# Kernel tuning notes

Hardware: AMD Instinct MI355X
Metric: run time of the kernel (lower is better)

## Reference

```python
import jax, jax.numpy as jnp
import numpy as np

H = 4096      # hidden_size (Llama-7B)
I = 11008     # intermediate_size (Llama-7B)
T = 4096      # tokens = batch 2 * seq 2048


def setup_inputs() -> dict:
    key = jax.random.key(0)
    ks = jax.random.split(key, 10)
    # int8 activations in [-128, 127]
    x = jax.random.randint(ks[0], (T, H), -128, 128, dtype=jnp.int32).astype(jnp.int8)
    # int4 weights stored as int8 values in [-8, 7], layout [out, in]
    gate_w = jax.random.randint(ks[1], (I, H), -8, 8, dtype=jnp.int32).astype(jnp.int8)
    up_w   = jax.random.randint(ks[2], (I, H), -8, 8, dtype=jnp.int32).astype(jnp.int8)
    down_w = jax.random.randint(ks[3], (H, I), -8, 8, dtype=jnp.int32).astype(jnp.int8)
    # per-output-channel dequant scale (input_scale * weight_scale) and fp32 bias
    gate_alpha = jax.random.uniform(ks[4], (I,), jnp.float32, 1e-4, 3e-4)
    up_alpha   = jax.random.uniform(ks[5], (I,), jnp.float32, 1e-4, 3e-4)
    down_alpha = jax.random.uniform(ks[6], (H,), jnp.float32, 1e-4, 3e-4)
    gate_bias = jax.random.normal(ks[7], (I,), jnp.float32) * 0.01
    up_bias   = jax.random.normal(ks[8], (I,), jnp.float32) * 0.01
    down_bias = jax.random.normal(ks[9], (H,), jnp.float32) * 0.01
    down_input_scale = jnp.array(0.1, dtype=jnp.float32)
    return dict(x=x, gate_w=gate_w, up_w=up_w, down_w=down_w,
                gate_alpha=gate_alpha, gate_bias=gate_bias,
                up_alpha=up_alpha, up_bias=up_bias,
                down_alpha=down_alpha, down_bias=down_bias,
                down_input_scale=down_input_scale)


def _w4a8_linear(x_i8, w_i4, alpha, bias):
    # int8 act x int4 weight -> int32 accumulate, per-out-channel dequant, fp32 out
    acc = jnp.matmul(x_i8.astype(jnp.int32), w_i4.T.astype(jnp.int32))  # [T, out]
    return acc.astype(jnp.float32) * alpha + bias


def reference(x, gate_w, up_w, down_w, gate_alpha, gate_bias, up_alpha, up_bias,
              down_alpha, down_bias, down_input_scale):
    g = _w4a8_linear(x, gate_w, gate_alpha, gate_bias)          # [T, I] fp32
    u = _w4a8_linear(x, up_w, up_alpha, up_bias)                # [T, I] fp32
    h = jax.nn.silu(g) * u                                      # SwiGLU
    # requantize to int8 for down_proj input (values kept exact as fp32)
    hq = jnp.clip(jnp.round(h / down_input_scale), -128.0, 127.0)
    out = jnp.matmul(hq, down_w.T.astype(jnp.float32)) * down_alpha + down_bias
    return out
```

## Files before the change

kernel.cpp:

```cpp
#include <hip/hip_runtime.h>
#include <stdint.h>

#define H_DIM 4096
#define I_DIM 11008
#define T_DIM 4096

typedef int i32x4 __attribute__((ext_vector_type(4)));
typedef const void __attribute__((address_space(1))) gvoid_t;
typedef void __attribute__((address_space(3))) svoid_t;

__device__ __forceinline__ void gload_lds16(const void* gsrc, void* ldst) {
    __builtin_amdgcn_global_load_lds((gvoid_t*)gsrc, (svoid_t*)ldst, 16, 0, 0);
}
__device__ __forceinline__ void wait_vmcnt6() {
    asm volatile("s_waitcnt vmcnt(6)" ::: "memory");
}
__device__ __forceinline__ void wait_vmcnt0() {
    asm volatile("s_waitcnt vmcnt(0)" ::: "memory");
}
__device__ __forceinline__ void wait_lgkm0() {
    asm volatile("s_waitcnt lgkmcnt(0)" ::: "memory");
    __builtin_amdgcn_sched_barrier(0);
}
__device__ __forceinline__ void barrier_() {
    asm volatile("s_barrier" ::: "memory");
}

__device__ __forceinline__ uint32_t pack4(int4 v) {
    uint32_t r = (uint32_t)(uint8_t)v.x;
    r |= (uint32_t)(uint8_t)v.y << 8;
    r |= (uint32_t)(uint8_t)v.z << 16;
    r |= (uint32_t)(uint8_t)v.w << 24;
    return r;
}

__global__ void convert_kernel(const int* __restrict__ src, int8_t* __restrict__ dst,
                               int n4) {
    int idx = blockIdx.x * blockDim.x + threadIdx.x;
    int stride = gridDim.x * blockDim.x;
    for (int i = idx; i < n4; i += stride) {
        int4 v = ((const int4*)src)[i];
        ((uint32_t*)dst)[i] = pack4(v);
    }
}

#define MFMA_I8 __builtin_amdgcn_mfma_i32_16x16x64_i8

__global__ __launch_bounds__(256, 2)
void gateup_kernel(const int8_t* __restrict__ x8, const int8_t* __restrict__ gw8,
                   const int8_t* __restrict__ uw8,
                   const float* __restrict__ galpha, const float* __restrict__ gbias,
                   const float* __restrict__ ualpha, const float* __restrict__ ubias,
                   const float* __restrict__ scale_p, int8_t* __restrict__ hq)
{
    __shared__ __align__(16) int8_t lsA[2][128 * 64];
    __shared__ __align__(16) int8_t lsG[2][128 * 64];
    __shared__ __align__(16) int8_t lsU[2][128 * 64];

    const int bid = blockIdx.x;
    const int mt = bid & 31;
    const int nt = bid >> 5;
    const int m0 = mt << 7;
    const int n0 = nt << 7;

    const int tid  = threadIdx.x;
    const int lane = tid & 63;
    const int wid  = tid >> 6;
    const int wr   = wid >> 1;
    const int wc   = wid & 1;
    const int lr   = lane & 15;
    const int rdsw = ((lane >> 4) ^ ((lr >> 1) & 3)) << 4;

    const int srow = tid >> 2;
    const int scol = ((tid & 3) ^ ((tid >> 3) & 3)) << 4;
    const int woff = wid << 10;

    const int8_t* As = x8  + (size_t)(m0 + srow) * H_DIM + scol;
    const int8_t* Gs = gw8 + (size_t)(n0 + srow) * H_DIM + scol;
    const int8_t* Us = uw8 + (size_t)(n0 + srow) * H_DIM + scol;

    i32x4 accg[4][4], accu[4][4];
#pragma unroll
    for (int mf = 0; mf < 4; ++mf)
#pragma unroll
        for (int nf = 0; nf < 4; ++nf) {
            accg[mf][nf] = i32x4{0, 0, 0, 0};
            accu[mf][nf] = i32x4{0, 0, 0, 0};
        }

    const int aro = (wr * 64 + lr) * 64 + rdsw;
    const int gro = (wc * 64 + lr) * 64 + rdsw;

#define STAGE_GU(b, kb) do { \
        gload_lds16(As + (kb),                        &lsA[b][woff]); \
        gload_lds16(As + (kb) + (size_t)64 * H_DIM,   &lsA[b][4096 + woff]); \
        gload_lds16(Gs + (kb),                        &lsG[b][woff]); \
        gload_lds16(Gs + (kb) + (size_t)64 * H_DIM,   &lsG[b][4096 + woff]); \
        gload_lds16(Us + (kb),                        &lsU[b][woff]); \
        gload_lds16(Us + (kb) + (size_t)64 * H_DIM,   &lsU[b][4096 + woff]); \
    } while (0)

    const int NKT = H_DIM / 64;
    STAGE_GU(0, 0);
    STAGE_GU(1, 64);

    for (int t = 0; t < NKT; ++t) {
        const int cur = t & 1;
        wait_vmcnt6();
        barrier_();
        i32x4 af[4], bg[4], bu[4];
#pragma unroll
        for (int mf = 0; mf < 4; ++mf) af[mf] = *(const i32x4*)&lsA[cur][aro + mf * 1024];
#pragma unroll
        for (int nf = 0; nf < 4; ++nf) {
            bg[nf] = *(const i32x4*)&lsG[cur][gro + nf * 1024];
            bu[nf] = *(const i32x4*)&lsU[cur][gro + nf * 1024];
        }
        wait_lgkm0();
        barrier_();
        {
            const int t2 = (t + 2 < NKT) ? (t + 2) : (t + 2 - NKT);
            STAGE_GU(cur, t2 * 64);
        }
#pragma unroll
        for (int mf = 0; mf < 4; ++mf)
#pragma unroll
            for (int nf = 0; nf < 4; ++nf) {
                accg[mf][nf] = MFMA_I8(af[mf], bg[nf], accg[mf][nf], 0, 0, 0);
                accu[mf][nf] = MFMA_I8(af[mf], bu[nf], accu[mf][nf], 0, 0, 0);
            }
    }
#undef STAGE_GU
    wait_vmcnt0();

    const float scale = *scale_p;
#pragma unroll
    for (int nf = 0; nf < 4; ++nf) {
        const int col = n0 + wc * 64 + nf * 16 + lr;
        const float gA = galpha[col], gB = gbias[col];
        const float uA = ualpha[col], uB = ubias[col];
#pragma unroll
        for (int mf = 0; mf < 4; ++mf) {
            const int row0 = m0 + wr * 64 + mf * 16 + (lane >> 4) * 4;
#pragma unroll
            for (int j = 0; j < 4; ++j) {
                float g = (float)accg[mf][nf][j] * gA + gB;
                float u = (float)accu[mf][nf][j] * uA + uB;
                float s = 1.0f / (1.0f + __expf(-g));
                float h = g * s * u;
                float q = rintf(h / scale);
                q = fminf(127.0f, fmaxf(-128.0f, q));
                hq[(size_t)(row0 + j) * I_DIM + col] = (int8_t)q;
            }
        }
    }
}

__global__ __launch_bounds__(256, 2)
void down_kernel(const int8_t* __restrict__ hq, const int8_t* __restrict__ dw8,
                 const float* __restrict__ dalpha, const float* __restrict__ dbias,
                 float* __restrict__ out)
{
    __shared__ __align__(16) int8_t lsA[2][256 * 64];
    __shared__ __align__(16) int8_t lsB[2][128 * 64];

    const int bid = blockIdx.x;
    const int mt = bid & 15;
    const int nt = bid >> 4;
    const int m0 = mt << 8;
    const int n0 = nt << 7;

    const int tid  = threadIdx.x;
    const int lane = tid & 63;
    const int wid  = tid >> 6;
    const int wr   = wid >> 1;
    const int wc   = wid & 1;
    const int lr   = lane & 15;
    const int rdsw = ((lane >> 4) ^ ((lr >> 1) & 3)) << 4;

    const int srow = tid >> 2;
    const int scol = ((tid & 3) ^ ((tid >> 3) & 3)) << 4;
    const int woff = wid << 10;

    const int8_t* Ap = hq  + (size_t)(m0 + srow) * I_DIM + scol;
    const int8_t* Bp = dw8 + (size_t)(n0 + srow) * I_DIM + scol;

    i32x4 acc[8][4];
#pragma unroll
    for (int mf = 0; mf < 8; ++mf)
#pragma unroll
        for (int nf = 0; nf < 4; ++nf) acc[mf][nf] = i32x4{0, 0, 0, 0};

    const int aro = (wr * 128 + lr) * 64 + rdsw;
    const int bro = (wc * 64 + lr) * 64 + rdsw;

#define STAGE_D(b, kb) do { \
        gload_lds16(Ap + (kb),                         &lsA[b][woff]); \
        gload_lds16(Ap + (kb) + (size_t)64 * I_DIM,    &lsA[b][4096 + woff]); \
        gload_lds16(Ap + (kb) + (size_t)128 * I_DIM,   &lsA[b][8192 + woff]); \
        gload_lds16(Ap + (kb) + (size_t)192 * I_DIM,   &lsA[b][12288 + woff]); \
        gload_lds16(Bp + (kb),                         &lsB[b][woff]); \
        gload_lds16(Bp + (kb) + (size_t)64 * I_DIM,    &lsB[b][4096 + woff]); \
    } while (0)

    const int NKT = I_DIM / 64;
    STAGE_D(0, 0);
    STAGE_D(1, 64);

    for (int t = 0; t < NKT; ++t) {
        const int cur = t & 1;
        wait_vmcnt6();
        barrier_();
        i32x4 af[8], bf[4];
#pragma unroll
        for (int mf = 0; mf < 8; ++mf) af[mf] = *(const i32x4*)&lsA[cur][aro + mf * 1024];
#pragma unroll
        for (int nf = 0; nf < 4; ++nf) bf[nf] = *(const i32x4*)&lsB[cur][bro + nf * 1024];
        wait_lgkm0();
        barrier_();
        {
            const int t2 = (t + 2 < NKT) ? (t + 2) : (t + 2 - NKT);
            STAGE_D(cur, t2 * 64);
        }
#pragma unroll
        for (int mf = 0; mf < 8; ++mf)
#pragma unroll
            for (int nf = 0; nf < 4; ++nf)
                acc[mf][nf] = MFMA_I8(af[mf], bf[nf], acc[mf][nf], 0, 0, 0);
    }
#undef STAGE_D
    wait_vmcnt0();

#pragma unroll
    for (int nf = 0; nf < 4; ++nf) {
        const int col = n0 + wc * 64 + nf * 16 + lr;
        const float dA = dalpha[col], dB = dbias[col];
#pragma unroll
        for (int mf = 0; mf < 8; ++mf) {
            const int row0 = m0 + wr * 128 + mf * 16 + (lane >> 4) * 4;
#pragma unroll
            for (int j = 0; j < 4; ++j) {
                out[(size_t)(row0 + j) * H_DIM + col] = (float)acc[mf][nf][j] * dA + dB;
            }
        }
    }
}

extern "C" void kernel_launch(void* const* d_in, const int* in_sizes, int n_in,
                              void* d_out, int out_size, void* d_ws, size_t ws_size,
                              hipStream_t stream) {
    const int* x32  = (const int*)d_in[0];
    const int* gw32 = (const int*)d_in[1];
    const int* uw32 = (const int*)d_in[2];
    const int* dw32 = (const int*)d_in[3];
    const float* ga = (const float*)d_in[4];
    const float* gb = (const float*)d_in[5];
    const float* ua = (const float*)d_in[6];
    const float* ub = (const float*)d_in[7];
    const float* da = (const float*)d_in[8];
    const float* db = (const float*)d_in[9];
    const float* sc = (const float*)d_in[10];
    float* out = (float*)d_out;

    const size_t SZ_X8 = (size_t)T_DIM * H_DIM;
    const size_t SZ_W  = (size_t)I_DIM * H_DIM;
    const size_t SZ_HQ = (size_t)T_DIM * I_DIM;

    int8_t* gw8 = (int8_t*)d_ws;
    int8_t* uw8 = gw8 + SZ_W;
    int8_t* hq  = uw8 + SZ_W;
    int8_t* x8  = hq + SZ_HQ;

    convert_kernel<<<dim3(2048), dim3(256), 0, stream>>>(x32, x8, (int)(SZ_X8 / 4));
    convert_kernel<<<dim3(2048), dim3(256), 0, stream>>>(gw32, gw8, (int)(SZ_W / 4));
    convert_kernel<<<dim3(2048), dim3(256), 0, stream>>>(uw32, uw8, (int)(SZ_W / 4));
    gateup_kernel<<<dim3(32 * 86), dim3(256), 0, stream>>>(
        x8, gw8, uw8, ga, gb, ua, ub, sc, hq);
    int8_t* dw8 = gw8;
    convert_kernel<<<dim3(2048), dim3(256), 0, stream>>>(dw32, dw8, (int)(SZ_W / 4));
    down_kernel<<<dim3(16 * 32), dim3(256), 0, stream>>>(hq, dw8, da, db, out);
}
```

Baseline: 732.8 us.

## Triple-buffer LDS and prefetch register fragments to cut barriers per k-step

Both GEMM kernels move from double to triple LDS buffering, with global loads issued three tiles ahead. The next tile's LDS fragments are read into a second register set while the current tile's MFMAs run, and the loop unrolls by two to alternate register sets. This drops one of two barriers per iteration and overlaps LDS reads with MFMA. In exchange, LDS per block grows by half (72KB for gateup, 72KB for down) and register use doubles for fragments, which may lower occupancy below two blocks per CU.

```diff
diff --git a/kernel.cpp b/kernel.cpp
--- a/kernel.cpp
+++ b/kernel.cpp
@@ -14,6 +14,9 @@
 }
 __device__ __forceinline__ void wait_vmcnt6() {
     asm volatile("s_waitcnt vmcnt(6)" ::: "memory");
+}
+__device__ __forceinline__ void wait_vmcnt12() {
+    asm volatile("s_waitcnt vmcnt(12)" ::: "memory");
 }
 __device__ __forceinline__ void wait_vmcnt0() {
     asm volatile("s_waitcnt vmcnt(0)" ::: "memory");
@@ -53,9 +56,9 @@
                    const float* __restrict__ ualpha, const float* __restrict__ ubias,
                    const float* __restrict__ scale_p, int8_t* __restrict__ hq)
 {
-    __shared__ __align__(16) int8_t lsA[2][128 * 64];
-    __shared__ __align__(16) int8_t lsG[2][128 * 64];
-    __shared__ __align__(16) int8_t lsU[2][128 * 64];
+    __shared__ __align__(16) int8_t lsA[3][128 * 64];
+    __shared__ __align__(16) int8_t lsG[3][128 * 64];
+    __shared__ __align__(16) int8_t lsU[3][128 * 64];
 
     const int bid = blockIdx.x;
     const int mt = bid & 31;
@@ -100,36 +103,43 @@
         gload_lds16(Us + (kb) + (size_t)64 * H_DIM,   &lsU[b][4096 + woff]); \
     } while (0)
 
+#define RD_GU(AF, BG, BU, tt) do { \
+        const int _b = (tt) % 3; \
+        _Pragma("unroll") for (int mf = 0; mf < 4; ++mf) \
+            AF[mf] = *(const i32x4*)&lsA[_b][aro + mf * 1024]; \
+        _Pragma("unroll") for (int nf = 0; nf < 4; ++nf) { \
+            BG[nf] = *(const i32x4*)&lsG[_b][gro + nf * 1024]; \
+            BU[nf] = *(const i32x4*)&lsU[_b][gro + nf * 1024]; } \
+    } while (0)
+
+#define STEP_GU(AF, BG, BU, AF2, BG2, BU2, tt) do { \
+        wait_vmcnt6(); \
+        wait_lgkm0(); \
+        barrier_(); \
+        STAGE_GU((tt) % 3, ((((tt) + 3) & (NKT - 1)) << 6)); \
+        RD_GU(AF2, BG2, BU2, (tt) + 1); \
+        _Pragma("unroll") for (int mf = 0; mf < 4; ++mf) \
+        _Pragma("unroll") for (int nf = 0; nf < 4; ++nf) { \
+            accg[mf][nf] = MFMA_I8(AF[mf], BG[nf], accg[mf][nf], 0, 0, 0); \
+            accu[mf][nf] = MFMA_I8(AF[mf], BU[nf], accu[mf][nf], 0, 0, 0); } \
+    } while (0)
+
     const int NKT = H_DIM / 64;
     STAGE_GU(0, 0);
     STAGE_GU(1, 64);
-
-    for (int t = 0; t < NKT; ++t) {
-        const int cur = t & 1;
-        wait_vmcnt6();
-        barrier_();
-        i32x4 af[4], bg[4], bu[4];
-#pragma unroll
-        for (int mf = 0; mf < 4; ++mf) af[mf] = *(const i32x4*)&lsA[cur][aro + mf * 1024];
-#pragma unroll
-        for (int nf = 0; nf < 4; ++nf) {
-            bg[nf] = *(const i32x4*)&lsG[cur][gro + nf * 1024];
-            bu[nf] = *(const i32x4*)&lsU[cur][gro + nf * 1024];
-        }
-        wait_lgkm0();
-        barrier_();
-        {
-            const int t2 = (t + 2 < NKT) ? (t + 2) : (t + 2 - NKT);
-            STAGE_GU(cur, t2 * 64);
-        }
-#pragma unroll
-        for (int mf = 0; mf < 4; ++mf)
-#pragma unroll
-            for (int nf = 0; nf < 4; ++nf) {
-                accg[mf][nf] = MFMA_I8(af[mf], bg[nf], accg[mf][nf], 0, 0, 0);
-                accu[mf][nf] = MFMA_I8(af[mf], bu[nf], accu[mf][nf], 0, 0, 0);
-            }
-    }
+    STAGE_GU(2, 128);
+    wait_vmcnt12();
+    barrier_();
+
+    i32x4 afA[4], bgA[4], buA[4], afB[4], bgB[4], buB[4];
+    RD_GU(afA, bgA, buA, 0);
+
+    for (int t = 0; t < NKT; t += 2) {
+        STEP_GU(afA, bgA, buA, afB, bgB, buB, t);
+        STEP_GU(afB, bgB, buB, afA, bgA, buA, t + 1);
+    }
+#undef STEP_GU
+#undef RD_GU
 #undef STAGE_GU
     wait_vmcnt0();
 
@@ -161,8 +171,8 @@
                  const float* __restrict__ dalpha, const float* __restrict__ dbias,
                  float* __restrict__ out)
 {
-    __shared__ __align__(16) int8_t lsA[2][256 * 64];
-    __shared__ __align__(16) int8_t lsB[2][128 * 64];
+    __shared__ __align__(16) int8_t lsA[3][256 * 64];
+    __shared__ __align__(16) int8_t lsB[3][128 * 64];
 
     const int bid = blockIdx.x;
     const int mt = bid & 15;
@@ -203,31 +213,41 @@
         gload_lds16(Bp + (kb) + (size_t)64 * I_DIM,    &lsB[b][4096 + woff]); \
     } while (0)
 
+#define RD_D(AF, BF, tt) do { \
+        const int _b = (tt) % 3; \
+        _Pragma("unroll") for (int mf = 0; mf < 8; ++mf) \
+            AF[mf] = *(const i32x4*)&lsA[_b][aro + mf * 1024]; \
+        _Pragma("unroll") for (int nf = 0; nf < 4; ++nf) \
+            BF[nf] = *(const i32x4*)&lsB[_b][bro + nf * 1024]; \
+    } while (0)
+
+#define STEP_D(AF, BF, AF2, BF2, tt) do { \
+        wait_vmcnt6(); \
+        wait_lgkm0(); \
+        barrier_(); \
+        { const int _t3 = ((tt) + 3) % NKT; STAGE_D((tt) % 3, _t3 << 6); } \
+        RD_D(AF2, BF2, (tt) + 1); \
+        _Pragma("unroll") for (int mf = 0; mf < 8; ++mf) \
+        _Pragma("unroll") for (int nf = 0; nf < 4; ++nf) \
+            acc[mf][nf] = MFMA_I8(AF[mf], BF[nf], acc[mf][nf], 0, 0, 0); \
+    } while (0)
+
     const int NKT = I_DIM / 64;
     STAGE_D(0, 0);
     STAGE_D(1, 64);
-
-    for (int t = 0; t < NKT; ++t) {
-        const int cur = t & 1;
-        wait_vmcnt6();
-        barrier_();
-        i32x4 af[8], bf[4];
-#pragma unroll
-        for (int mf = 0; mf < 8; ++mf) af[mf] = *(const i32x4*)&lsA[cur][aro + mf * 1024];
-#pragma unroll
-        for (int nf = 0; nf < 4; ++nf) bf[nf] = *(const i32x4*)&lsB[cur][bro + nf * 1024];
-        wait_lgkm0();
-        barrier_();
-        {
-            const int t2 = (t + 2 < NKT) ? (t + 2) : (t + 2 - NKT);
-            STAGE_D(cur, t2 * 64);
-        }
-#pragma unroll
-        for (int mf = 0; mf < 8; ++mf)
-#pragma unroll
-            for (int nf = 0; nf < 4; ++nf)
-                acc[mf][nf] = MFMA_I8(af[mf], bf[nf], acc[mf][nf], 0, 0, 0);
-    }
+    STAGE_D(2, 128);
+    wait_vmcnt12();
+    barrier_();
+
+    i32x4 afA[8], bfA[4], afB[8], bfB[4];
+    RD_D(afA, bfA, 0);
+
+    for (int t = 0; t < NKT; t += 2) {
+        STEP_D(afA, bfA, afB, bfB, t);
+        STEP_D(afB, bfB, afA, bfA, t + 1);
+    }
+#undef STEP_D
+#undef RD_D
 #undef STAGE_D
     wait_vmcnt0();
 
```

Measured after the change: 736.2 us. About the same (+0.5%).

## Use 8-wave blocks with gate/up split across waves and reshaped down tiles

Applied to the files above, without the earlier changes.

Both GEMM kernels go from 4 to 8 waves per block. In gate/up, half the waves compute the gate product and half the up product, and the up accumulators pass through LDS for the SwiGLU epilogue. The down kernel switches to 128x256 tiles split over 2x4 waves, with fewer accumulators per wave. The aim is to cut per-thread register pressure and add latency hiding through more waves, at the cost of an extra LDS round trip and barriers in the gate/up epilogue.

```diff
diff --git a/kernel.cpp b/kernel.cpp
--- a/kernel.cpp
+++ b/kernel.cpp
@@ -12,8 +12,8 @@
 __device__ __forceinline__ void gload_lds16(const void* gsrc, void* ldst) {
     __builtin_amdgcn_global_load_lds((gvoid_t*)gsrc, (svoid_t*)ldst, 16, 0, 0);
 }
-__device__ __forceinline__ void wait_vmcnt6() {
-    asm volatile("s_waitcnt vmcnt(6)" ::: "memory");
+__device__ __forceinline__ void wait_vmcnt3() {
+    asm volatile("s_waitcnt vmcnt(3)" ::: "memory");
 }
 __device__ __forceinline__ void wait_vmcnt0() {
     asm volatile("s_waitcnt vmcnt(0)" ::: "memory");
@@ -46,16 +46,17 @@
 
 #define MFMA_I8 __builtin_amdgcn_mfma_i32_16x16x64_i8
 
-__global__ __launch_bounds__(256, 2)
+__global__ __launch_bounds__(512, 4)
 void gateup_kernel(const int8_t* __restrict__ x8, const int8_t* __restrict__ gw8,
                    const int8_t* __restrict__ uw8,
                    const float* __restrict__ galpha, const float* __restrict__ gbias,
                    const float* __restrict__ ualpha, const float* __restrict__ ubias,
                    const float* __restrict__ scale_p, int8_t* __restrict__ hq)
 {
-    __shared__ __align__(16) int8_t lsA[2][128 * 64];
-    __shared__ __align__(16) int8_t lsG[2][128 * 64];
-    __shared__ __align__(16) int8_t lsU[2][128 * 64];
+    __shared__ __align__(16) int8_t smem_s[49152];
+    int8_t* lsA = smem_s;
+    int8_t* lsG = smem_s + 16384;
+    int8_t* lsU = smem_s + 32768;
 
     const int bid = blockIdx.x;
     const int mt = bid & 31;
@@ -66,8 +67,10 @@
     const int tid  = threadIdx.x;
     const int lane = tid & 63;
     const int wid  = tid >> 6;
-    const int wr   = wid >> 1;
-    const int wc   = wid & 1;
+    const int isU  = wid >> 2;
+    const int w4   = wid & 3;
+    const int wr   = w4 >> 1;
+    const int wc   = w4 & 1;
     const int lr   = lane & 15;
     const int rdsw = ((lane >> 4) ^ ((lr >> 1) & 3)) << 4;
 
@@ -79,102 +82,111 @@
     const int8_t* Gs = gw8 + (size_t)(n0 + srow) * H_DIM + scol;
     const int8_t* Us = uw8 + (size_t)(n0 + srow) * H_DIM + scol;
 
-    i32x4 accg[4][4], accu[4][4];
+    i32x4 acc[4][4];
 #pragma unroll
     for (int mf = 0; mf < 4; ++mf)
 #pragma unroll
-        for (int nf = 0; nf < 4; ++nf) {
-            accg[mf][nf] = i32x4{0, 0, 0, 0};
-            accu[mf][nf] = i32x4{0, 0, 0, 0};
-        }
+        for (int nf = 0; nf < 4; ++nf) acc[mf][nf] = i32x4{0, 0, 0, 0};
 
     const int aro = (wr * 64 + lr) * 64 + rdsw;
-    const int gro = (wc * 64 + lr) * 64 + rdsw;
-
-#define STAGE_GU(b, kb) do { \
-        gload_lds16(As + (kb),                        &lsA[b][woff]); \
-        gload_lds16(As + (kb) + (size_t)64 * H_DIM,   &lsA[b][4096 + woff]); \
-        gload_lds16(Gs + (kb),                        &lsG[b][woff]); \
-        gload_lds16(Gs + (kb) + (size_t)64 * H_DIM,   &lsG[b][4096 + woff]); \
-        gload_lds16(Us + (kb),                        &lsU[b][woff]); \
-        gload_lds16(Us + (kb) + (size_t)64 * H_DIM,   &lsU[b][4096 + woff]); \
+    const int bro = (wc * 64 + lr) * 64 + rdsw;
+    const int8_t* myB = isU ? lsU : lsG;
+
+#define STAGE3(b, kb) do { \
+        gload_lds16(As + (kb), lsA + (b) * 8192 + woff); \
+        gload_lds16(Gs + (kb), lsG + (b) * 8192 + woff); \
+        gload_lds16(Us + (kb), lsU + (b) * 8192 + woff); \
     } while (0)
 
     const int NKT = H_DIM / 64;
-    STAGE_GU(0, 0);
-    STAGE_GU(1, 64);
+    STAGE3(0, 0);
+    STAGE3(1, 64);
 
     for (int t = 0; t < NKT; ++t) {
         const int cur = t & 1;
-        wait_vmcnt6();
-        barrier_();
-        i32x4 af[4], bg[4], bu[4];
-#pragma unroll
-        for (int mf = 0; mf < 4; ++mf) af[mf] = *(const i32x4*)&lsA[cur][aro + mf * 1024];
-#pragma unroll
-        for (int nf = 0; nf < 4; ++nf) {
-            bg[nf] = *(const i32x4*)&lsG[cur][gro + nf * 1024];
-            bu[nf] = *(const i32x4*)&lsU[cur][gro + nf * 1024];
-        }
+        wait_vmcnt3();
+        barrier_();
+        i32x4 af[4], bf[4];
+#pragma unroll
+        for (int mf = 0; mf < 4; ++mf)
+            af[mf] = *(const i32x4*)(lsA + cur * 8192 + aro + mf * 1024);
+#pragma unroll
+        for (int nf = 0; nf < 4; ++nf)
+            bf[nf] = *(const i32x4*)(myB + cur * 8192 + bro + nf * 1024);
         wait_lgkm0();
         barrier_();
-        {
-            const int t2 = (t + 2 < NKT) ? (t + 2) : (t + 2 - NKT);
-            STAGE_GU(cur, t2 * 64);
-        }
-#pragma unroll
-        for (int mf = 0; mf < 4; ++mf)
-#pragma unroll
-            for (int nf = 0; nf < 4; ++nf) {
-                accg[mf][nf] = MFMA_I8(af[mf], bg[nf], accg[mf][nf], 0, 0, 0);
-                accu[mf][nf] = MFMA_I8(af[mf], bu[nf], accu[mf][nf], 0, 0, 0);
+        STAGE3(cur, ((t + 2) & (NKT - 1)) << 6);
+#pragma unroll
+        for (int mf = 0; mf < 4; ++mf)
+#pragma unroll
+            for (int nf = 0; nf < 4; ++nf)
+                acc[mf][nf] = MFMA_I8(af[mf], bf[nf], acc[mf][nf], 0, 0, 0);
+    }
+#undef STAGE3
+    wait_vmcnt0();
+    barrier_();
+
+    const float scale = *scale_p;
+#pragma unroll
+    for (int h = 0; h < 2; ++h) {
+        if (isU) {
+#pragma unroll
+            for (int mf = 0; mf < 4; ++mf)
+#pragma unroll
+                for (int q = 0; q < 2; ++q)
+                    *(i32x4*)(smem_s + w4 * 8192 + mf * 2048 + q * 1024 + lane * 16)
+                        = acc[mf][h * 2 + q];
+        }
+        barrier_();
+        if (!isU) {
+#pragma unroll
+            for (int q = 0; q < 2; ++q) {
+                const int nf = h * 2 + q;
+                const int col = n0 + wc * 64 + nf * 16 + lr;
+                const float gA = galpha[col], gB = gbias[col];
+                const float uA = ualpha[col], uB = ubias[col];
+#pragma unroll
+                for (int mf = 0; mf < 4; ++mf) {
+                    i32x4 uacc = *(const i32x4*)(smem_s + w4 * 8192 + mf * 2048
+                                                 + q * 1024 + lane * 16);
+                    const int row0 = m0 + wr * 64 + mf * 16 + (lane >> 4) * 4;
+#pragma unroll
+                    for (int j = 0; j < 4; ++j) {
+                        float g = (float)acc[mf][nf][j] * gA + gB;
+                        float u = (float)uacc[j] * uA + uB;
+                        float s = 1.0f / (1.0f + __expf(-g));
+                        float hh = g * s * u;
+                        float qv = rintf(hh / scale);
+                        qv = fminf(127.0f, fmaxf(-128.0f, qv));
+                        hq[(size_t)(row0 + j) * I_DIM + col] = (int8_t)qv;
+                    }
+                }
             }
-    }
-#undef STAGE_GU
-    wait_vmcnt0();
-
-    const float scale = *scale_p;
-#pragma unroll
-    for (int nf = 0; nf < 4; ++nf) {
-        const int col = n0 + wc * 64 + nf * 16 + lr;
-        const float gA = galpha[col], gB = gbias[col];
-        const float uA = ualpha[col], uB = ubias[col];
-#pragma unroll
-        for (int mf = 0; mf < 4; ++mf) {
-            const int row0 = m0 + wr * 64 + mf * 16 + (lane >> 4) * 4;
-#pragma unroll
-            for (int j = 0; j < 4; ++j) {
-                float g = (float)accg[mf][nf][j] * gA + gB;
-                float u = (float)accu[mf][nf][j] * uA + uB;
-                float s = 1.0f / (1.0f + __expf(-g));
-                float h = g * s * u;
-                float q = rintf(h / scale);
-                q = fminf(127.0f, fmaxf(-128.0f, q));
-                hq[(size_t)(row0 + j) * I_DIM + col] = (int8_t)q;
-            }
-        }
-    }
-}
-
-__global__ __launch_bounds__(256, 2)
+        }
+        barrier_();
+    }
+}
+
+__global__ __launch_bounds__(512, 4)
 void down_kernel(const int8_t* __restrict__ hq, const int8_t* __restrict__ dw8,
                  const float* __restrict__ dalpha, const float* __restrict__ dbias,
                  float* __restrict__ out)
 {
-    __shared__ __align__(16) int8_t lsA[2][256 * 64];
-    __shared__ __align__(16) int8_t lsB[2][128 * 64];
+    __shared__ __align__(16) int8_t smem_d[49152];
+    int8_t* lsA = smem_d;
+    int8_t* lsB = smem_d + 16384;
 
     const int bid = blockIdx.x;
-    const int mt = bid & 15;
-    const int nt = bid >> 4;
-    const int m0 = mt << 8;
-    const int n0 = nt << 7;
+    const int mt = bid & 31;
+    const int nt = bid >> 5;
+    const int m0 = mt << 7;
+    const int n0 = nt << 8;
 
     const int tid  = threadIdx.x;
     const int lane = tid & 63;
     const int wid  = tid >> 6;
-    const int wr   = wid >> 1;
-    const int wc   = wid & 1;
+    const int wr   = wid >> 2;
+    const int wc   = wid & 3;
     const int lr   = lane & 15;
     const int rdsw = ((lane >> 4) ^ ((lr >> 1) & 3)) << 4;
 
@@ -185,50 +197,49 @@
     const int8_t* Ap = hq  + (size_t)(m0 + srow) * I_DIM + scol;
     const int8_t* Bp = dw8 + (size_t)(n0 + srow) * I_DIM + scol;
 
-    i32x4 acc[8][4];
-#pragma unroll
-    for (int mf = 0; mf < 8; ++mf)
+    i32x4 acc[4][4];
+#pragma unroll
+    for (int mf = 0; mf < 4; ++mf)
 #pragma unroll
         for (int nf = 0; nf < 4; ++nf) acc[mf][nf] = i32x4{0, 0, 0, 0};
 
-    const int aro = (wr * 128 + lr) * 64 + rdsw;
+    const int aro = (wr * 64 + lr) * 64 + rdsw;
     const int bro = (wc * 64 + lr) * 64 + rdsw;
 
-#define STAGE_D(b, kb) do { \
-        gload_lds16(Ap + (kb),                         &lsA[b][woff]); \
-        gload_lds16(Ap + (kb) + (size_t)64 * I_DIM,    &lsA[b][4096 + woff]); \
-        gload_lds16(Ap + (kb) + (size_t)128 * I_DIM,   &lsA[b][8192 + woff]); \
-        gload_lds16(Ap + (kb) + (size_t)192 * I_DIM,   &lsA[b][12288 + woff]); \
-        gload_lds16(Bp + (kb),                         &lsB[b][woff]); \
-        gload_lds16(Bp + (kb) + (size_t)64 * I_DIM,    &lsB[b][4096 + woff]); \
+#define STAGE3(b, kb) do { \
+        gload_lds16(Ap + (kb), lsA + (b) * 8192 + woff); \
+        gload_lds16(Bp + (kb), lsB + (b) * 16384 + woff); \
+        gload_lds16(Bp + (kb) + (size_t)128 * I_DIM, lsB + (b) * 16384 + 8192 + woff); \
     } while (0)
 
     const int NKT = I_DIM / 64;
-    STAGE_D(0, 0);
-    STAGE_D(1, 64);
+    STAGE3(0, 0);
+    STAGE3(1, 64);
 
     for (int t = 0; t < NKT; ++t) {
         const int cur = t & 1;
-        wait_vmcnt6();
-        barrier_();
-        i32x4 af[8], bf[4];
-#pragma unroll
-        for (int mf = 0; mf < 8; ++mf) af[mf] = *(const i32x4*)&lsA[cur][aro + mf * 1024];
-#pragma unroll
-        for (int nf = 0; nf < 4; ++nf) bf[nf] = *(const i32x4*)&lsB[cur][bro + nf * 1024];
+        wait_vmcnt3();
+        barrier_();
+        i32x4 af[4], bf[4];
+#pragma unroll
+        for (int mf = 0; mf < 4; ++mf)
+            af[mf] = *(const i32x4*)(lsA + cur * 8192 + aro + mf * 1024);
+#pragma unroll
+        for (int nf = 0; nf < 4; ++nf)
+            bf[nf] = *(const i32x4*)(lsB + cur * 16384 + bro + nf * 1024);
         wait_lgkm0();
         barrier_();
         {
             const int t2 = (t + 2 < NKT) ? (t + 2) : (t + 2 - NKT);
-            STAGE_D(cur, t2 * 64);
-        }
-#pragma unroll
-        for (int mf = 0; mf < 8; ++mf)
+            STAGE3(cur, t2 * 64);
+        }
+#pragma unroll
+        for (int mf = 0; mf < 4; ++mf)
 #pragma unroll
             for (int nf = 0; nf < 4; ++nf)
                 acc[mf][nf] = MFMA_I8(af[mf], bf[nf], acc[mf][nf], 0, 0, 0);
     }
-#undef STAGE_D
+#undef STAGE3
     wait_vmcnt0();
 
 #pragma unroll
@@ -236,8 +247,8 @@
         const int col = n0 + wc * 64 + nf * 16 + lr;
         const float dA = dalpha[col], dB = dbias[col];
 #pragma unroll
-        for (int mf = 0; mf < 8; ++mf) {
-            const int row0 = m0 + wr * 128 + mf * 16 + (lane >> 4) * 4;
+        for (int mf = 0; mf < 4; ++mf) {
+            const int row0 = m0 + wr * 64 + mf * 16 + (lane >> 4) * 4;
 #pragma unroll
             for (int j = 0; j < 4; ++j) {
                 out[(size_t)(row0 + j) * H_DIM + col] = (float)acc[mf][nf][j] * dA + dB;
@@ -274,9 +285,9 @@
     convert_kernel<<<dim3(2048), dim3(256), 0, stream>>>(x32, x8, (int)(SZ_X8 / 4));
     convert_kernel<<<dim3(2048), dim3(256), 0, stream>>>(gw32, gw8, (int)(SZ_W / 4));
     convert_kernel<<<dim3(2048), dim3(256), 0, stream>>>(uw32, uw8, (int)(SZ_W / 4));
-    gateup_kernel<<<dim3(32 * 86), dim3(256), 0, stream>>>(
+    gateup_kernel<<<dim3(32 * 86), dim3(512), 0, stream>>>(
         x8, gw8, uw8, ga, gb, ua, ub, sc, hq);
     int8_t* dw8 = gw8;
     convert_kernel<<<dim3(2048), dim3(256), 0, stream>>>(dw32, dw8, (int)(SZ_W / 4));
-    down_kernel<<<dim3(16 * 32), dim3(256), 0, stream>>>(hq, dw8, da, db, out);
-}
+    down_kernel<<<dim3(32 * 16), dim3(512), 0, stream>>>(hq, dw8, da, db, out);
+}
```

Result: faster. 715.1 us (-2.4%).
